# Kernel optimization log

Measured on AMD Instinct MI355X. Metric: run time of the kernel, lower is better.

## Reference

```python
import jax, jax.numpy as jnp
import numpy as np

NUM_HEADS = 8
EPS_OT = 0.05    # self.eps
BETA_T = 1.0     # self.beta_t
N_ITERS = 100    # Sinkhorn max_iter (reference runs all iterations; torch breaks early on convergence)


def setup_inputs() -> dict:
    key = jax.random.key(0)
    ks = jax.random.split(key, 10)
    B, N1, N2 = 16, 256, 576
    dim_t, dim_v, dim_out = 512, 512, 512
    s = 0.02  # conv1d k=1 init scale (stand-in for torch default init)
    f32 = jnp.float32
    return {
        "F_t": jax.random.normal(ks[0], (B, N1, dim_t), f32),
        "F_s": jax.random.normal(ks[1], (B, N2, dim_v), f32),
        # Conv1d(kernel_size=1) weights, squeezed to [out, in]; biases default-on in nn.Conv1d
        "Wq": jax.random.normal(ks[2], (dim_out, dim_t), f32) * s,
        "bq": jnp.zeros((dim_out,), f32),
        "Wk": jax.random.normal(ks[3], (dim_out, dim_v), f32) * s,
        "bk": jnp.zeros((dim_out,), f32),
        "Wv": jax.random.normal(ks[4], (dim_out, dim_v), f32) * s,
        "bv": jnp.zeros((dim_out,), f32),
        "Wp": jax.random.normal(ks[5], (dim_out, dim_out), f32) * s,
        "bp": jnp.zeros((dim_out,), f32),
    }


def sinkhorn_log_exp_sum(C, log_mu, log_nu, eps):
    # C: [BH, N1, N2]; fixed-length log-domain Sinkhorn.
    BH, N1, N2 = C.shape
    u0 = jnp.zeros((BH, N1), C.dtype)
    v0 = jnp.zeros((BH, N2), C.dtype)

    def body(carry, _):
        u, v = carry
        # single K per iteration; both u and v updates use the OLD (u, v), matching torch code
        K = (-C + u[:, :, None] + v[:, None, :]) / eps
        u_new = eps * (log_mu - jax.scipy.special.logsumexp(K, axis=2)) + u
        v_new = eps * (log_nu - jax.scipy.special.logsumexp(K, axis=1)) + v
        return (u_new, v_new), None

    (u, v), _ = jax.lax.scan(jax.checkpoint(body), (u0, v0), None, length=N_ITERS)
    return jnp.exp((-C + u[:, :, None] + v[:, None, :]) / eps)


def _l2norm(x, eps=1e-12):
    return x / jnp.maximum(jnp.linalg.norm(x, axis=-1, keepdims=True), eps)


def reference(F_t, F_s, Wq, bq, Wk, bk, Wv, bv, Wp, bp):
    B, N1, _ = F_t.shape
    N2 = F_s.shape[1]
    H = NUM_HEADS
    dim_out = Wq.shape[0]
    hd = dim_out // H

    # Conv1d(kernel=1) == pointwise linear over channel dim
    q = (F_t @ Wq.T + bq).reshape(B, N1, H, hd)
    k = (F_s @ Wk.T + bk).reshape(B, N2, H, hd)
    v = (F_s @ Wv.T + bv).reshape(B, N2, H, hd)

    q = _l2norm(q)
    k = _l2norm(k)

    sim = jnp.einsum('bnkc,bmkc->bknm', q, k) * BETA_T  # [B,H,N1,N2]
    wdist = (1.0 - sim).reshape(B * H, N1, N2)
    sim_f = sim.reshape(B * H, N1, N2)

    log_mu = jnp.log(jnp.asarray(1.0 / N1 + 1e-8, sim.dtype))
    log_nu = jnp.log(jnp.asarray(1.0 / N2 + 1e-8, sim.dtype))
    T = sinkhorn_log_exp_sum(wdist, log_mu, log_nu, EPS_OT)

    score_map = (N1 * N2 * sim_f * T).reshape(B, H, N1, N2)  # attn_drop = identity (p=0)
    F_t_a = jnp.einsum('bknm,bmkc->bnkc', score_map, v).reshape(B, N1, dim_out)
    F_t_a = F_t_a @ Wp.T + bp
    # torch: F_t_a / F_t_a.norm(dim=-1, keepdim=True)  (plain division, no eps clamp)
    F_t_a = F_t_a / jnp.linalg.norm(F_t_a, axis=-1, keepdims=True)
    return F_t_a  # proj_drop = identity (p=0)
```

## Files before the change

kernel.cpp:

```cpp
#include <hip/hip_runtime.h>
#include <math.h>

#define EPS_OT 0.05f
#define INV_EPS 20.0f

typedef unsigned short ushort_t;
typedef __attribute__((ext_vector_type(8))) short short8;
typedef __attribute__((ext_vector_type(4))) float f32x4;
union Pk { uint4 u; short8 s; };

__device__ __forceinline__ unsigned int f2bf(float f) {
  unsigned int u = __float_as_uint(f);
  return (u + 0x7FFFu + ((u >> 16) & 1u)) >> 16;
}
__device__ __forceinline__ float bf2f(unsigned int u) { return __uint_as_float(u << 16); }

__global__ __launch_bounds__(256) void pack_k(const float* __restrict__ F_t,
                                              const float* __restrict__ F_s,
                                              const float* __restrict__ Wq,
                                              const float* __restrict__ Wk,
                                              const float* __restrict__ Wv,
                                              const float* __restrict__ Wp,
                                              ushort_t* __restrict__ Fth, ushort_t* __restrict__ Ftl,
                                              ushort_t* __restrict__ Fsh, ushort_t* __restrict__ Fsl,
                                              ushort_t* __restrict__ Wqh, ushort_t* __restrict__ Wql,
                                              ushort_t* __restrict__ Wkh, ushort_t* __restrict__ Wkl,
                                              ushort_t* __restrict__ Wvh, ushort_t* __restrict__ Wvl,
                                              ushort_t* __restrict__ Wph) {
  const int blk = blockIdx.x;
  const float* src; ushort_t* dh; ushort_t* dl; size_t off;
  if (blk < 2048)      { src = F_t; dh = Fth; dl = Ftl; off = (size_t)blk * 1024; }
  else if (blk < 6656) { src = F_s; dh = Fsh; dl = Fsl; off = (size_t)(blk - 2048) * 1024; }
  else if (blk < 6912) { src = Wq;  dh = Wqh; dl = Wql; off = (size_t)(blk - 6656) * 1024; }
  else if (blk < 7168) { src = Wk;  dh = Wkh; dl = Wkl; off = (size_t)(blk - 6912) * 1024; }
  else if (blk < 7424) { src = Wv;  dh = Wvh; dl = Wvl; off = (size_t)(blk - 7168) * 1024; }
  else                 { src = Wp;  dh = Wph; dl = nullptr; off = (size_t)(blk - 7424) * 1024; }
  const size_t i = off + (size_t)threadIdx.x * 4;
  float4 f = *(const float4*)(src + i);
  unsigned int h0 = f2bf(f.x), h1 = f2bf(f.y), h2 = f2bf(f.z), h3 = f2bf(f.w);
  uint2 hh; hh.x = h0 | (h1 << 16); hh.y = h2 | (h3 << 16);
  *(uint2*)(dh + i) = hh;
  if (dl) {
    uint2 ll;
    ll.x = f2bf(f.x - bf2f(h0)) | (f2bf(f.y - bf2f(h1)) << 16);
    ll.y = f2bf(f.z - bf2f(h2)) | (f2bf(f.w - bf2f(h3)) << 16);
    *(uint2*)(dl + i) = ll;
  }
}

#define GEMM_HL_BODY()                                                                      \
  f32x4 acc[4] = {};                                                                        \
  for (int k0 = 0; k0 < 512; k0 += 64) {                                                    \
    uint4 a0 = *(const uint4*)(Xp_h + k0), a1 = *(const uint4*)(Xp_h + k0 + 8);             \
    uint4 b0 = *(const uint4*)(Xp_l + k0), b1 = *(const uint4*)(Xp_l + k0 + 8);             \
    uint4 c0 = *(const uint4*)(Wp_h + k0), c1 = *(const uint4*)(Wp_h + k0 + 8);             \
    uint4 d0 = *(const uint4*)(Wp_l + k0), d1 = *(const uint4*)(Wp_l + k0 + 8);             \
    __syncthreads();                                                                        \
    *(uint4*)&Xh[r][cg * 16] = a0; *(uint4*)&Xh[r][cg * 16 + 8] = a1;                       \
    *(uint4*)&Xl[r][cg * 16] = b0; *(uint4*)&Xl[r][cg * 16 + 8] = b1;                       \
    *(uint4*)&Wh[r][cg * 16] = c0; *(uint4*)&Wh[r][cg * 16 + 8] = c1;                       \
    *(uint4*)&Wl[r][cg * 16] = d0; *(uint4*)&Wl[r][cg * 16 + 8] = d1;                       \
    __syncthreads();                                                                        \
    _Pragma("unroll") for (int kst = 0; kst < 2; ++kst) {                                   \
      short8 ah = *(const short8*)&Xh[16 * w + li][kst * 32 + 8 * lg];                      \
      short8 al = *(const short8*)&Xl[16 * w + li][kst * 32 + 8 * lg];                      \
      _Pragma("unroll") for (int nt = 0; nt < 4; ++nt) {                                    \
        short8 bh = *(const short8*)&Wh[nt * 16 + li][kst * 32 + 8 * lg];                   \
        short8 bl = *(const short8*)&Wl[nt * 16 + li][kst * 32 + 8 * lg];                   \
        acc[nt] = __builtin_amdgcn_mfma_f32_16x16x32_bf16(ah, bh, acc[nt], 0, 0, 0);        \
        acc[nt] = __builtin_amdgcn_mfma_f32_16x16x32_bf16(ah, bl, acc[nt], 0, 0, 0);        \
        acc[nt] = __builtin_amdgcn_mfma_f32_16x16x32_bf16(al, bh, acc[nt], 0, 0, 0);        \
      }                                                                                     \
    }                                                                                       \
  }

#define GEMM_PL_BODY()                                                                      \
  f32x4 acc[4] = {};                                                                        \
  for (int k0 = 0; k0 < 512; k0 += 64) {                                                    \
    uint4 a0 = *(const uint4*)(Xp_h + k0), a1 = *(const uint4*)(Xp_h + k0 + 8);             \
    uint4 c0 = *(const uint4*)(Wp_h + k0), c1 = *(const uint4*)(Wp_h + k0 + 8);             \
    __syncthreads();                                                                        \
    *(uint4*)&Xh[r][cg * 16] = a0; *(uint4*)&Xh[r][cg * 16 + 8] = a1;                       \
    *(uint4*)&Wh[r][cg * 16] = c0; *(uint4*)&Wh[r][cg * 16 + 8] = c1;                       \
    __syncthreads();                                                                        \
    _Pragma("unroll") for (int kst = 0; kst < 2; ++kst) {                                   \
      short8 ah = *(const short8*)&Xh[16 * w + li][kst * 32 + 8 * lg];                      \
      _Pragma("unroll") for (int nt = 0; nt < 4; ++nt) {                                    \
        short8 bh = *(const short8*)&Wh[nt * 16 + li][kst * 32 + 8 * lg];                   \
        acc[nt] = __builtin_amdgcn_mfma_f32_16x16x32_bf16(ah, bh, acc[nt], 0, 0, 0);        \
      }                                                                                     \
    }                                                                                       \
  }

__global__ __launch_bounds__(256) void gemmnorm2_k(const ushort_t* __restrict__ Xg_h,
                                                   const ushort_t* __restrict__ Xg_l,
                                                   const ushort_t* __restrict__ Wg_h,
                                                   const ushort_t* __restrict__ Wg_l,
                                                   const float* __restrict__ bias,
                                                   ushort_t* __restrict__ oh,
                                                   ushort_t* __restrict__ ol, int Nn) {
  __shared__ ushort_t Xh[64][72], Xl[64][72], Wh[64][72], Wl[64][72];
  const int tid = threadIdx.x;
  const int w = tid >> 6, l = tid & 63, li = l & 15, lg = l >> 4;
  const int r = tid >> 2, cg = tid & 3;
  const int m0 = blockIdx.x << 6;
  const int h = blockIdx.y, n0 = h << 6;
  const ushort_t* Xp_h = Xg_h + (size_t)(m0 + r) * 512 + cg * 16;
  const ushort_t* Xp_l = Xg_l + (size_t)(m0 + r) * 512 + cg * 16;
  const ushort_t* Wp_h = Wg_h + (size_t)(n0 + r) * 512 + cg * 16;
  const ushort_t* Wp_l = Wg_l + (size_t)(n0 + r) * 512 + cg * 16;
  GEMM_HL_BODY()
  float v[4][4];
  float ss[4] = {0.f, 0.f, 0.f, 0.f};
#pragma unroll
  for (int nt = 0; nt < 4; ++nt) {
    float bb = bias[n0 + nt * 16 + li];
#pragma unroll
    for (int reg = 0; reg < 4; ++reg) {
      float y = acc[nt][reg] + bb;
      v[nt][reg] = y;
      ss[reg] = fmaf(y, y, ss[reg]);
    }
  }
#pragma unroll
  for (int off = 1; off < 16; off <<= 1)
#pragma unroll
    for (int reg = 0; reg < 4; ++reg) ss[reg] += __shfl_xor(ss[reg], off, 64);
  const int b = m0 / Nn;
  const int nbase = m0 - b * Nn;
  const size_t base = ((size_t)(b * 8 + h) * Nn + nbase + 16 * w + 4 * lg) * 64;
#pragma unroll
  for (int reg = 0; reg < 4; ++reg) {
    float inv = 1.0f / fmaxf(sqrtf(ss[reg]), 1e-12f);
#pragma unroll
    for (int nt = 0; nt < 4; ++nt) {
      float y = v[nt][reg] * inv;
      unsigned int hi = f2bf(y);
      size_t idx = base + (size_t)reg * 64 + nt * 16 + li;
      oh[idx] = (ushort_t)hi;
      ol[idx] = (ushort_t)f2bf(y - bf2f(hi));
    }
  }
}

__global__ __launch_bounds__(256) void gemmtrans2_k(const ushort_t* __restrict__ Xg_h,
                                                    const ushort_t* __restrict__ Wg_h,
                                                    const float* __restrict__ bias,
                                                    ushort_t* __restrict__ vt) {
  __shared__ ushort_t Xh[64][72], Wh[64][72];
  __shared__ ushort_t Vs[64 * 73];
  const int tid = threadIdx.x;
  const int w = tid >> 6, l = tid & 63, li = l & 15, lg = l >> 4;
  const int r = tid >> 2, cg = tid & 3;
  const int m0 = blockIdx.x << 6;
  const int h = blockIdx.y, n0 = h << 6;
  const ushort_t* Xp_h = Xg_h + (size_t)(m0 + r) * 512 + cg * 16;
  const ushort_t* Wp_h = Wg_h + (size_t)(n0 + r) * 512 + cg * 16;
  GEMM_PL_BODY()
#pragma unroll
  for (int nt = 0; nt < 4; ++nt) {
    float bb = bias[n0 + nt * 16 + li];
#pragma unroll
    for (int reg = 0; reg < 4; ++reg)
      Vs[(16 * w + 4 * lg + reg) * 73 + nt * 16 + li] = (ushort_t)f2bf(acc[nt][reg] + bb);
  }
  __syncthreads();
  const int a9 = m0 >> 6;
  const int b = a9 / 9;
  const int nbase = m0 - b * 576;
  const int s = b * 8 + h;
  const int c = tid >> 2, q4 = tid & 3;
  ushort_t tmp[16];
#pragma unroll
  for (int jj = 0; jj < 16; ++jj) tmp[jj] = Vs[(q4 * 16 + jj) * 73 + c];
  ushort_t* op = vt + ((size_t)s * 64 + c) * 576 + nbase + q4 * 16;
  *(uint4*)op = *(uint4*)&tmp[0];
  *(uint4*)(op + 8) = *(uint4*)&tmp[8];
}

__global__ __launch_bounds__(256) void gemmplain_k(const ushort_t* __restrict__ Xg_h,
                                                   const ushort_t* __restrict__ Wg_h,
                                                   const float* __restrict__ bias,
                                                   float* __restrict__ Y) {
  __shared__ ushort_t Xh[64][72], Wh[64][72];
  const int tid = threadIdx.x;
  const int w = tid >> 6, l = tid & 63, li = l & 15, lg = l >> 4;
  const int r = tid >> 2, cg = tid & 3;
  const int m0 = blockIdx.x << 6, n0 = blockIdx.y << 6;
  const ushort_t* Xp_h = Xg_h + (size_t)(m0 + r) * 512 + cg * 16;
  const ushort_t* Wp_h = Wg_h + (size_t)(n0 + r) * 512 + cg * 16;
  GEMM_PL_BODY()
#pragma unroll
  for (int nt = 0; nt < 4; ++nt) {
    float bb = bias[n0 + nt * 16 + li];
#pragma unroll
    for (int reg = 0; reg < 4; ++reg)
      Y[(size_t)(m0 + 16 * w + 4 * lg + reg) * 512 + n0 + nt * 16 + li] = acc[nt][reg] + bb;
  }
}

__global__ __launch_bounds__(256) void simE2_k(const ushort_t* __restrict__ qh,
                                               const ushort_t* __restrict__ ql,
                                               const ushort_t* __restrict__ kh,
                                               const ushort_t* __restrict__ kl,
                                               ushort_t* __restrict__ E) {
  const int s = blockIdx.x, i0 = blockIdx.y << 6, j0 = blockIdx.z << 6;
  const int tid = threadIdx.x;
  const int w = tid >> 6, l = tid & 63, li = l & 15, lg = l >> 4;
  const size_t qoff = ((size_t)s * 256 + i0 + 16 * w + li) * 64 + 8 * lg;
  short8 aH0 = *(const short8*)(qh + qoff), aH1 = *(const short8*)(qh + qoff + 32);
  short8 aL0 = *(const short8*)(ql + qoff), aL1 = *(const short8*)(ql + qoff + 32);
  f32x4 acc[4] = {};
#pragma unroll
  for (int nt = 0; nt < 4; ++nt) {
    const size_t koff = ((size_t)s * 576 + j0 + nt * 16 + li) * 64 + 8 * lg;
    short8 bH0 = *(const short8*)(kh + koff), bH1 = *(const short8*)(kh + koff + 32);
    short8 bL0 = *(const short8*)(kl + koff), bL1 = *(const short8*)(kl + koff + 32);
    acc[nt] = __builtin_amdgcn_mfma_f32_16x16x32_bf16(aH0, bH0, acc[nt], 0, 0, 0);
    acc[nt] = __builtin_amdgcn_mfma_f32_16x16x32_bf16(aH1, bH1, acc[nt], 0, 0, 0);
    acc[nt] = __builtin_amdgcn_mfma_f32_16x16x32_bf16(aH0, bL0, acc[nt], 0, 0, 0);
    acc[nt] = __builtin_amdgcn_mfma_f32_16x16x32_bf16(aH1, bL1, acc[nt], 0, 0, 0);
    acc[nt] = __builtin_amdgcn_mfma_f32_16x16x32_bf16(aL0, bH0, acc[nt], 0, 0, 0);
    acc[nt] = __builtin_amdgcn_mfma_f32_16x16x32_bf16(aL1, bH1, acc[nt], 0, 0, 0);
  }
  ushort_t* Ep = E + (size_t)s * 147456;
#pragma unroll
  for (int nt = 0; nt < 4; ++nt)
#pragma unroll
    for (int reg = 0; reg < 4; ++reg) {
      float e = __expf((acc[nt][reg] - 1.0f) * INV_EPS);
      Ep[(size_t)(i0 + 16 * w + 4 * lg + reg) * 576 + j0 + nt * 16 + li] = (ushort_t)f2bf(e);
    }
}

#define SK_SMEM 147456

__global__ __launch_bounds__(1024, 1) void sinkhorn6_k(const ushort_t* __restrict__ E,
                                                       float* __restrict__ gA,
                                                       float* __restrict__ gB,
                                                       unsigned long long* __restrict__ gpart,
                                                       float C_mu, float C_nu) {
  extern __shared__ char smem[];
  const int g = blockIdx.x, s = g >> 1, rh = g & 1, pg = g ^ 1;
  const int tid = threadIdx.x, w = tid >> 6, l = tid & 63, li = l & 15, lg = l >> 4;
  unsigned long long* myP = gpart + (size_t)g * 1152;
  const unsigned long long* prP = gpart + (size_t)pg * 1152;

  ushort_t* Elds = (ushort_t*)smem;
  {
    const uint4* Eg = (const uint4*)(E + (size_t)s * 147456 + (size_t)rh * 73728);
    uint4* El4 = (uint4*)Elds;
    for (int idx = tid; idx < 9216; idx += 1024) El4[idx] = Eg[idx];
  }
  __syncthreads();

  short8 afr[9];
#pragma unroll
  for (int rt = 0; rt < 8; ++rt)
    afr[rt] = *(const short8*)(Elds + (rt * 16 + li) * 576 + w * 32 + 8 * lg);
  const int rtx = w & 7, ktx = 16 + (w >> 3);
  afr[8] = *(const short8*)(Elds + (rtx * 16 + li) * 576 + ktx * 32 + 8 * lg);
  const int ktB = w >> 2, ntb = (w & 3) * 9;
  short8 bfr[9];
#pragma unroll
  for (int p9 = 0; p9 < 9; ++p9) {
    const ushort_t* p = Elds + (ktB * 32 + 8 * lg) * 576 + (ntb + p9) * 16 + li;
    Pk pk;
    pk.u.x = (unsigned int)p[0]    | ((unsigned int)p[576]  << 16);
    pk.u.y = (unsigned int)p[1152] | ((unsigned int)p[1728] << 16);
    pk.u.z = (unsigned int)p[2304] | ((unsigned int)p[2880] << 16);
    pk.u.w = (unsigned int)p[3456] | ((unsigned int)p[4032] << 16);
    bfr[p9] = pk.s;
  }
  __syncthreads();

  float* uu = (float*)smem;
  float* vv = uu + 128;
  unsigned int* au_h = (unsigned int*)(vv + 576);
  unsigned int* au_l = au_h + 64;
  unsigned int* bv_h = au_l + 64;
  unsigned int* bv_l = bv_h + 288;
  float* rpart = (float*)(bv_l + 288);
  float* colp = rpart + 2304;
  float* cso = colp + 2304;
  ushort_t* au_hs = (ushort_t*)au_h;
  ushort_t* au_ls = (ushort_t*)au_l;
  ushort_t* bv_hs = (ushort_t*)bv_h;
  ushort_t* bv_ls = (ushort_t*)bv_l;

  if (tid < 64) { au_h[tid] = 0x3F803F80u; au_l[tid] = 0u; }
  if (tid < 288) { bv_h[tid] = 0x3F803F80u; bv_l[tid] = 0u; }
  __syncthreads();

  for (int t = 0; t < 100; ++t) {
    {
      Pk ah, al;
      ah.u = *(const uint4*)&au_h[ktB * 16 + 4 * lg];
      al.u = *(const uint4*)&au_l[ktB * 16 + 4 * lg];
      float* cp = colp + (w >> 2) * 576;
#pragma unroll
      for (int p9 = 0; p9 < 9; ++p9) {
        f32x4 a2 = {0.f, 0.f, 0.f, 0.f};
        a2 = __builtin_amdgcn_mfma_f32_16x16x32_bf16(ah.s, bfr[p9], a2, 0, 0, 0);
        a2 = __builtin_amdgcn_mfma_f32_16x16x32_bf16(al.s, bfr[p9], a2, 0, 0, 0);
        if (l < 16) cp[(ntb + p9) * 16 + l] = a2[0];
      }
    }
    __syncthreads();
    const int par = t & 1;
    if (tid < 576) {
      float cs = colp[tid] + colp[576 + tid] + colp[1152 + tid] + colp[1728 + tid];
      cso[tid] = cs;
      unsigned long long pv = (unsigned long long)__float_as_uint(cs) |
                              ((unsigned long long)(unsigned int)(t + 1) << 32);
      __hip_atomic_store(&myP[par * 576 + tid], pv, __ATOMIC_RELAXED, __HIP_MEMORY_SCOPE_AGENT);
    }
    {
      Pk bh, bl, bhx, blx;
      bh.u = *(const uint4*)&bv_h[w * 16 + 4 * lg];
      bl.u = *(const uint4*)&bv_l[w * 16 + 4 * lg];
      bhx.u = *(const uint4*)&bv_h[ktx * 16 + 4 * lg];
      blx.u = *(const uint4*)&bv_l[ktx * 16 + 4 * lg];
#pragma unroll
      for (int rt = 0; rt < 8; ++rt) {
        f32x4 a1 = {0.f, 0.f, 0.f, 0.f};
        a1 = __builtin_amdgcn_mfma_f32_16x16x32_bf16(bh.s, afr[rt], a1, 0, 0, 0);
        a1 = __builtin_amdgcn_mfma_f32_16x16x32_bf16(bl.s, afr[rt], a1, 0, 0, 0);
        if (l < 16) rpart[w * 128 + rt * 16 + l] = a1[0];
      }
      f32x4 a1 = {0.f, 0.f, 0.f, 0.f};
      a1 = __builtin_amdgcn_mfma_f32_16x16x32_bf16(bhx.s, afr[8], a1, 0, 0, 0);
      a1 = __builtin_amdgcn_mfma_f32_16x16x32_bf16(blx.s, afr[8], a1, 0, 0, 0);
      if (l < 16) rpart[ktx * 128 + rtx * 16 + l] = a1[0];
    }
    __syncthreads();
    if (tid < 128) {
      float rs = 0.0f;
#pragma unroll
      for (int kc = 0; kc < 18; ++kc) rs += rpart[kc * 128 + tid];
      float un = C_mu - EPS_OT * __logf(rs);
      uu[tid] = un;
      float a = __expf(fminf(fmaxf(un * INV_EPS, -80.f), 80.f));
      unsigned int hi = f2bf(a);
      au_hs[tid] = (ushort_t)hi;
      au_ls[tid] = (ushort_t)f2bf(a - bf2f(hi));
    } else if (tid < 704) {
      const int j = tid - 128;
      const unsigned int tg = (unsigned int)(t + 1);
      unsigned long long p0;
      for (;;) {
        p0 = __hip_atomic_load(&prP[par * 576 + j], __ATOMIC_RELAXED, __HIP_MEMORY_SCOPE_AGENT);
        if ((unsigned int)(p0 >> 32) == tg) break;
        __builtin_amdgcn_s_sleep(1);
      }
      float tot = cso[j] + __uint_as_float((unsigned int)p0);
      float vn = C_nu - EPS_OT * __logf(tot);
      vv[j] = vn;
      float bb = __expf(fminf(fmaxf(vn * INV_EPS, -80.f), 80.f));
      unsigned int hi = f2bf(bb);
      bv_hs[j] = (ushort_t)hi;
      bv_ls[j] = (ushort_t)f2bf(bb - bf2f(hi));
    }
    __syncthreads();
  }
  if (tid < 128) gA[(size_t)s * 256 + rh * 128 + tid] = uu[tid] * INV_EPS;
  if (rh == 0 && tid < 576) gB[(size_t)s * 576 + tid] = vv[tid] * INV_EPS + 11.9012851f;
}

__global__ __launch_bounds__(256) void scorev2_k(const ushort_t* __restrict__ E,
                                                 const ushort_t* __restrict__ vt,
                                                 const float* __restrict__ gA,
                                                 const float* __restrict__ gB,
                                                 ushort_t* __restrict__ Y) {
  __shared__ float gBs[576];
  const int s = blockIdx.x, i0 = blockIdx.y << 6;
  const int tid = threadIdx.x;
  const int w = tid >> 6, l = tid & 63, li = l & 15, lg = l >> 4;
  for (int j = tid; j < 576; j += 256) gBs[j] = gB[(size_t)s * 576 + j];
  const float ga = gA[(size_t)s * 256 + i0 + 16 * w + li];
  const ushort_t* Erow = E + (size_t)s * 147456 + (size_t)(i0 + 16 * w + li) * 576;
  f32x4 acc[4] = {};
  __syncthreads();
  for (int kst = 0; kst < 18; ++kst) {
    const int jb = kst * 32 + 8 * lg;
    Pk eu; eu.u = *(const uint4*)(Erow + jb);
    float pv[8], pl8[8];
#pragma unroll
    for (int jj = 0; jj < 8; ++jj) {
      unsigned int us = (unsigned int)(unsigned short)eu.s[jj];
      float e = bf2f(us);
      float le = __logf(e);
      pv[jj] = (1.0f + EPS_OT * le) * __expf(le + ga + gBs[jb + jj]);
    }
    Pk ph, pl;
#pragma unroll
    for (int jj = 0; jj < 8; ++jj) {
      unsigned int h = f2bf(pv[jj]);
      ((unsigned short*)&ph.s)[jj] = (unsigned short)h;
      pl8[jj] = pv[jj] - bf2f(h);
    }
#pragma unroll
    for (int jj = 0; jj < 8; ++jj)
      ((unsigned short*)&pl.s)[jj] = (unsigned short)f2bf(pl8[jj]);
#pragma unroll
    for (int nt = 0; nt < 4; ++nt) {
      Pk vf; vf.u = *(const uint4*)(vt + ((size_t)s * 64 + nt * 16 + li) * 576 + jb);
      acc[nt] = __builtin_amdgcn_mfma_f32_16x16x32_bf16(ph.s, vf.s, acc[nt], 0, 0, 0);
      acc[nt] = __builtin_amdgcn_mfma_f32_16x16x32_bf16(pl.s, vf.s, acc[nt], 0, 0, 0);
    }
  }
  const int b = s >> 3, h = s & 7;
#pragma unroll
  for (int nt = 0; nt < 4; ++nt)
#pragma unroll
    for (int reg = 0; reg < 4; ++reg)
      Y[((size_t)(b * 256 + i0 + 16 * w + 4 * lg + reg) << 9) + (h << 6) + nt * 16 + li] =
          (ushort_t)f2bf(acc[nt][reg]);
}

__global__ __launch_bounds__(256) void rownorm_k(const float* __restrict__ X,
                                                 float* __restrict__ out) {
  const size_t row = blockIdx.x;
  const int tid = threadIdx.x;
  float x0 = X[(row << 9) + tid], x1 = X[(row << 9) + 256 + tid];
  float st = fmaf(x0, x0, x1 * x1);
#pragma unroll
  for (int off = 32; off; off >>= 1) st += __shfl_xor(st, off, 64);
  __shared__ float ps[4];
  if ((tid & 63) == 0) ps[tid >> 6] = st;
  __syncthreads();
  const float inv = 1.0f / sqrtf(ps[0] + ps[1] + ps[2] + ps[3]);
  out[(row << 9) + tid] = x0 * inv;
  out[(row << 9) + 256 + tid] = x1 * inv;
}

extern "C" void kernel_launch(void* const* d_in, const int* in_sizes, int n_in,
                              void* d_out, int out_size, void* d_ws, size_t ws_size,
                              hipStream_t stream) {
  const float* F_t = (const float*)d_in[0];
  const float* F_s = (const float*)d_in[1];
  const float* Wq = (const float*)d_in[2];
  const float* bq = (const float*)d_in[3];
  const float* Wk = (const float*)d_in[4];
  const float* bk = (const float*)d_in[5];
  const float* Wv = (const float*)d_in[6];
  const float* bvb = (const float*)d_in[7];
  const float* Wp = (const float*)d_in[8];
  const float* bp = (const float*)d_in[9];
  float* out = (float*)d_out;

  ushort_t* u0 = (ushort_t*)d_ws;
  ushort_t* Fth = u0;
  ushort_t* Ftl = Fth + 2097152;
  ushort_t* Fsh = Ftl + 2097152;
  ushort_t* Fsl = Fsh + 4718592;
  ushort_t* Wqh = Fsl + 4718592;
  ushort_t* Wql = Wqh + 262144;
  ushort_t* Wkh = Wql + 262144;
  ushort_t* Wkl = Wkh + 262144;
  ushort_t* Wvh = Wkl + 262144;
  ushort_t* Wvl = Wvh + 262144;
  ushort_t* Wph = Wvl + 262144;
  ushort_t* qh = Wph + 262144;
  ushort_t* ql = qh + 2097152;
  ushort_t* kh = ql + 2097152;
  ushort_t* kl = kh + 4718592;
  ushort_t* vt = kl + 4718592;
  ushort_t* Eb = vt + 4718592;
  ushort_t* T0b = Eb + 18874368;
  float* T1 = (float*)(T0b + 2097152);
  float* gA = T1 + 2097152;
  float* gB = gA + 32768;
  unsigned long long* gpart = (unsigned long long*)(gB + 73728);

  const float C_mu = (float)(0.05 * log(1.0 / 256.0 + 1e-8));
  const float C_nu = (float)(0.05 * log(1.0 / 576.0 + 1e-8));

  (void)hipFuncSetAttribute((const void*)sinkhorn6_k,
                            hipFuncAttributeMaxDynamicSharedMemorySize, SK_SMEM);

  pack_k<<<7680, 256, 0, stream>>>(F_t, F_s, Wq, Wk, Wv, Wp, Fth, Ftl, Fsh, Fsl,
                                   Wqh, Wql, Wkh, Wkl, Wvh, Wvl, Wph);
  gemmnorm2_k<<<dim3(64, 8), 256, 0, stream>>>(Fth, Ftl, Wqh, Wql, bq, qh, ql, 256);
  gemmnorm2_k<<<dim3(144, 8), 256, 0, stream>>>(Fsh, Fsl, Wkh, Wkl, bk, kh, kl, 576);
  gemmtrans2_k<<<dim3(144, 8), 256, 0, stream>>>(Fsh, Wvh, bvb, vt);
  simE2_k<<<dim3(128, 4, 9), 256, 0, stream>>>(qh, ql, kh, kl, Eb);
  sinkhorn6_k<<<256, 1024, SK_SMEM, stream>>>(Eb, gA, gB, gpart, C_mu, C_nu);
  scorev2_k<<<dim3(128, 4), 256, 0, stream>>>(Eb, vt, gA, gB, T0b);
  gemmplain_k<<<dim3(64, 8), 256, 0, stream>>>(T0b, Wph, bp, T1);
  rownorm_k<<<4096, 256, 0, stream>>>(T1, out);
}
```

Measured before the change: 430.3 us.

## Fuse similarity, Sinkhorn and score-V into one persistent kernel

```diff
diff --git a/kernel.cpp b/kernel.cpp
--- a/kernel.cpp
+++ b/kernel.cpp
@@ -199,60 +199,67 @@
   }
 }
 
-__global__ __launch_bounds__(256) void simE2_k(const ushort_t* __restrict__ qh,
-                                               const ushort_t* __restrict__ ql,
-                                               const ushort_t* __restrict__ kh,
-                                               const ushort_t* __restrict__ kl,
-                                               ushort_t* __restrict__ E) {
-  const int s = blockIdx.x, i0 = blockIdx.y << 6, j0 = blockIdx.z << 6;
-  const int tid = threadIdx.x;
-  const int w = tid >> 6, l = tid & 63, li = l & 15, lg = l >> 4;
-  const size_t qoff = ((size_t)s * 256 + i0 + 16 * w + li) * 64 + 8 * lg;
-  short8 aH0 = *(const short8*)(qh + qoff), aH1 = *(const short8*)(qh + qoff + 32);
-  short8 aL0 = *(const short8*)(ql + qoff), aL1 = *(const short8*)(ql + qoff + 32);
-  f32x4 acc[4] = {};
-#pragma unroll
-  for (int nt = 0; nt < 4; ++nt) {
-    const size_t koff = ((size_t)s * 576 + j0 + nt * 16 + li) * 64 + 8 * lg;
-    short8 bH0 = *(const short8*)(kh + koff), bH1 = *(const short8*)(kh + koff + 32);
-    short8 bL0 = *(const short8*)(kl + koff), bL1 = *(const short8*)(kl + koff + 32);
-    acc[nt] = __builtin_amdgcn_mfma_f32_16x16x32_bf16(aH0, bH0, acc[nt], 0, 0, 0);
-    acc[nt] = __builtin_amdgcn_mfma_f32_16x16x32_bf16(aH1, bH1, acc[nt], 0, 0, 0);
-    acc[nt] = __builtin_amdgcn_mfma_f32_16x16x32_bf16(aH0, bL0, acc[nt], 0, 0, 0);
-    acc[nt] = __builtin_amdgcn_mfma_f32_16x16x32_bf16(aH1, bL1, acc[nt], 0, 0, 0);
-    acc[nt] = __builtin_amdgcn_mfma_f32_16x16x32_bf16(aL0, bH0, acc[nt], 0, 0, 0);
-    acc[nt] = __builtin_amdgcn_mfma_f32_16x16x32_bf16(aL1, bH1, acc[nt], 0, 0, 0);
-  }
-  ushort_t* Ep = E + (size_t)s * 147456;
-#pragma unroll
-  for (int nt = 0; nt < 4; ++nt)
-#pragma unroll
-    for (int reg = 0; reg < 4; ++reg) {
-      float e = __expf((acc[nt][reg] - 1.0f) * INV_EPS);
-      Ep[(size_t)(i0 + 16 * w + 4 * lg + reg) * 576 + j0 + nt * 16 + li] = (ushort_t)f2bf(e);
-    }
-}
-
-#define SK_SMEM 147456
-
-__global__ __launch_bounds__(1024, 1) void sinkhorn6_k(const ushort_t* __restrict__ E,
-                                                       float* __restrict__ gA,
-                                                       float* __restrict__ gB,
+#define SK7_SMEM 155648
+
+__global__ __launch_bounds__(1024, 1) void sinkhorn7_k(const ushort_t* __restrict__ qh,
+                                                       const ushort_t* __restrict__ ql,
+                                                       const ushort_t* __restrict__ kh,
+                                                       const ushort_t* __restrict__ kl,
+                                                       const ushort_t* __restrict__ vt,
+                                                       ushort_t* __restrict__ Y,
                                                        unsigned long long* __restrict__ gpart,
                                                        float C_mu, float C_nu) {
   extern __shared__ char smem[];
+  ushort_t* Elds = (ushort_t*)smem;
+  char* scr = smem + 147456;
+  ushort_t* khs = (ushort_t*)scr;
+  ushort_t* kls = khs + 2048;
+  float* uu = (float*)scr;
+  float* vv = uu + 128;
+  float* rsum = vv + 576;
+  float* colsum = rsum + 128;
+  ushort_t* au = (ushort_t*)(colsum + 576);
+  ushort_t* bv = au + 128;
+
   const int g = blockIdx.x, s = g >> 1, rh = g & 1, pg = g ^ 1;
   const int tid = threadIdx.x, w = tid >> 6, l = tid & 63, li = l & 15, lg = l >> 4;
   unsigned long long* myP = gpart + (size_t)g * 1152;
   const unsigned long long* prP = gpart + (size_t)pg * 1152;
 
-  ushort_t* Elds = (ushort_t*)smem;
-  {
-    const uint4* Eg = (const uint4*)(E + (size_t)s * 147456 + (size_t)rh * 73728);
-    uint4* El4 = (uint4*)Elds;
-    for (int idx = tid; idx < 9216; idx += 1024) El4[idx] = Eg[idx];
-  }
-  __syncthreads();
+  const int it = w & 7, ntp = w >> 3;
+  const size_t qoff = ((size_t)(s * 256 + rh * 128 + it * 16 + li)) * 64 + 8 * lg;
+  short8 aH0 = *(const short8*)(qh + qoff), aH1 = *(const short8*)(qh + qoff + 32);
+  short8 aL0 = *(const short8*)(ql + qoff), aL1 = *(const short8*)(ql + qoff + 32);
+
+  for (int jt = 0; jt < 9; ++jt) {
+#pragma unroll
+    for (int p = 0; p < 2; ++p) {
+      const int q = tid & 511;
+      const int jr = jt * 64 + p * 32 + (q >> 4);
+      const size_t src = ((size_t)(s * 576 + jr)) * 64 + (q & 15) * 4;
+      if (tid < 512) ((uint2*)khs)[q] = *(const uint2*)(kh + src);
+      else           ((uint2*)kls)[q] = *(const uint2*)(kl + src);
+      __syncthreads();
+      const ushort_t* kb_h = khs + (ntp * 16 + li) * 64 + 8 * lg;
+      const ushort_t* kb_l = kls + (ntp * 16 + li) * 64 + 8 * lg;
+      short8 bH0 = *(const short8*)kb_h, bH1 = *(const short8*)(kb_h + 32);
+      short8 bL0 = *(const short8*)kb_l, bL1 = *(const short8*)(kb_l + 32);
+      f32x4 acc = {0.f, 0.f, 0.f, 0.f};
+      acc = __builtin_amdgcn_mfma_f32_16x16x32_bf16(aH0, bH0, acc, 0, 0, 0);
+      acc = __builtin_amdgcn_mfma_f32_16x16x32_bf16(aH1, bH1, acc, 0, 0, 0);
+      acc = __builtin_amdgcn_mfma_f32_16x16x32_bf16(aH0, bL0, acc, 0, 0, 0);
+      acc = __builtin_amdgcn_mfma_f32_16x16x32_bf16(aH1, bL1, acc, 0, 0, 0);
+      acc = __builtin_amdgcn_mfma_f32_16x16x32_bf16(aL0, bH0, acc, 0, 0, 0);
+      acc = __builtin_amdgcn_mfma_f32_16x16x32_bf16(aL1, bH1, acc, 0, 0, 0);
+#pragma unroll
+      for (int reg = 0; reg < 4; ++reg) {
+        float e = __expf((acc[reg] - 1.0f) * INV_EPS);
+        Elds[(it * 16 + 4 * lg + reg) * 576 + jt * 64 + p * 32 + ntp * 16 + li] =
+            (ushort_t)f2bf(e);
+      }
+      __syncthreads();
+    }
+  }
 
   short8 afr[9];
 #pragma unroll
@@ -272,150 +279,108 @@
     pk.u.w = (unsigned int)p[3456] | ((unsigned int)p[4032] << 16);
     bfr[p9] = pk.s;
   }
+  if (tid < 128) { uu[tid] = 0.0f; au[tid] = (ushort_t)0x3F80; rsum[tid] = 0.0f; }
+  if (tid < 576) { vv[tid] = 0.0f; bv[tid] = (ushort_t)0x3F80; colsum[tid] = 0.0f; }
   __syncthreads();
 
-  float* uu = (float*)smem;
-  float* vv = uu + 128;
-  unsigned int* au_h = (unsigned int*)(vv + 576);
-  unsigned int* au_l = au_h + 64;
-  unsigned int* bv_h = au_l + 64;
-  unsigned int* bv_l = bv_h + 288;
-  float* rpart = (float*)(bv_l + 288);
-  float* colp = rpart + 2304;
-  float* cso = colp + 2304;
-  ushort_t* au_hs = (ushort_t*)au_h;
-  ushort_t* au_ls = (ushort_t*)au_l;
-  ushort_t* bv_hs = (ushort_t*)bv_h;
-  ushort_t* bv_ls = (ushort_t*)bv_l;
-
-  if (tid < 64) { au_h[tid] = 0x3F803F80u; au_l[tid] = 0u; }
-  if (tid < 288) { bv_h[tid] = 0x3F803F80u; bv_l[tid] = 0u; }
-  __syncthreads();
-
   for (int t = 0; t < 100; ++t) {
+    if (tid < 128) rsum[tid] = 0.0f;
     {
-      Pk ah, al;
-      ah.u = *(const uint4*)&au_h[ktB * 16 + 4 * lg];
-      al.u = *(const uint4*)&au_l[ktB * 16 + 4 * lg];
-      float* cp = colp + (w >> 2) * 576;
+      Pk ah; ah.u = *(const uint4*)(au + ktB * 32 + 8 * lg);
 #pragma unroll
       for (int p9 = 0; p9 < 9; ++p9) {
         f32x4 a2 = {0.f, 0.f, 0.f, 0.f};
         a2 = __builtin_amdgcn_mfma_f32_16x16x32_bf16(ah.s, bfr[p9], a2, 0, 0, 0);
-        a2 = __builtin_amdgcn_mfma_f32_16x16x32_bf16(al.s, bfr[p9], a2, 0, 0, 0);
-        if (l < 16) cp[(ntb + p9) * 16 + l] = a2[0];
+        if (l < 16) atomicAdd(&colsum[(ntb + p9) * 16 + l], a2[0]);
       }
     }
     __syncthreads();
     const int par = t & 1;
+    float csMine = 0.0f;
     if (tid < 576) {
-      float cs = colp[tid] + colp[576 + tid] + colp[1152 + tid] + colp[1728 + tid];
-      cso[tid] = cs;
-      unsigned long long pv = (unsigned long long)__float_as_uint(cs) |
+      csMine = colsum[tid];
+      unsigned long long pv = (unsigned long long)__float_as_uint(csMine) |
                               ((unsigned long long)(unsigned int)(t + 1) << 32);
       __hip_atomic_store(&myP[par * 576 + tid], pv, __ATOMIC_RELAXED, __HIP_MEMORY_SCOPE_AGENT);
     }
     {
-      Pk bh, bl, bhx, blx;
-      bh.u = *(const uint4*)&bv_h[w * 16 + 4 * lg];
-      bl.u = *(const uint4*)&bv_l[w * 16 + 4 * lg];
-      bhx.u = *(const uint4*)&bv_h[ktx * 16 + 4 * lg];
-      blx.u = *(const uint4*)&bv_l[ktx * 16 + 4 * lg];
+      Pk bh, bhx;
+      bh.u = *(const uint4*)(bv + w * 32 + 8 * lg);
+      bhx.u = *(const uint4*)(bv + ktx * 32 + 8 * lg);
 #pragma unroll
       for (int rt = 0; rt < 8; ++rt) {
         f32x4 a1 = {0.f, 0.f, 0.f, 0.f};
         a1 = __builtin_amdgcn_mfma_f32_16x16x32_bf16(bh.s, afr[rt], a1, 0, 0, 0);
-        a1 = __builtin_amdgcn_mfma_f32_16x16x32_bf16(bl.s, afr[rt], a1, 0, 0, 0);
-        if (l < 16) rpart[w * 128 + rt * 16 + l] = a1[0];
+        if (l < 16) atomicAdd(&rsum[rt * 16 + l], a1[0]);
       }
       f32x4 a1 = {0.f, 0.f, 0.f, 0.f};
       a1 = __builtin_amdgcn_mfma_f32_16x16x32_bf16(bhx.s, afr[8], a1, 0, 0, 0);
-      a1 = __builtin_amdgcn_mfma_f32_16x16x32_bf16(blx.s, afr[8], a1, 0, 0, 0);
-      if (l < 16) rpart[ktx * 128 + rtx * 16 + l] = a1[0];
+      if (l < 16) atomicAdd(&rsum[rtx * 16 + l], a1[0]);
     }
     __syncthreads();
-    if (tid < 128) {
-      float rs = 0.0f;
-#pragma unroll
-      for (int kc = 0; kc < 18; ++kc) rs += rpart[kc * 128 + tid];
-      float un = C_mu - EPS_OT * __logf(rs);
-      uu[tid] = un;
-      float a = __expf(fminf(fmaxf(un * INV_EPS, -80.f), 80.f));
-      unsigned int hi = f2bf(a);
-      au_hs[tid] = (ushort_t)hi;
-      au_ls[tid] = (ushort_t)f2bf(a - bf2f(hi));
-    } else if (tid < 704) {
-      const int j = tid - 128;
+    if (tid < 576) {
       const unsigned int tg = (unsigned int)(t + 1);
       unsigned long long p0;
       for (;;) {
-        p0 = __hip_atomic_load(&prP[par * 576 + j], __ATOMIC_RELAXED, __HIP_MEMORY_SCOPE_AGENT);
+        p0 = __hip_atomic_load(&prP[par * 576 + tid], __ATOMIC_RELAXED, __HIP_MEMORY_SCOPE_AGENT);
         if ((unsigned int)(p0 >> 32) == tg) break;
         __builtin_amdgcn_s_sleep(1);
       }
-      float tot = cso[j] + __uint_as_float((unsigned int)p0);
-      float vn = C_nu - EPS_OT * __logf(tot);
-      vv[j] = vn;
-      float bb = __expf(fminf(fmaxf(vn * INV_EPS, -80.f), 80.f));
-      unsigned int hi = f2bf(bb);
-      bv_hs[j] = (ushort_t)hi;
-      bv_ls[j] = (ushort_t)f2bf(bb - bf2f(hi));
+      float vn = C_nu - EPS_OT * __logf(csMine + __uint_as_float((unsigned int)p0));
+      vv[tid] = vn;
+      bv[tid] = (ushort_t)f2bf(__expf(fminf(fmaxf(vn * INV_EPS, -80.f), 80.f)));
+    } else if (tid < 704) {
+      const int i = tid - 576;
+      float un = C_mu - EPS_OT * __logf(rsum[i]);
+      uu[i] = un;
+      au[i] = (ushort_t)f2bf(__expf(fminf(fmaxf(un * INV_EPS, -80.f), 80.f)));
+    } else {
+      for (int j = tid - 704; j < 576; j += 320) colsum[j] = 0.0f;
     }
     __syncthreads();
   }
-  if (tid < 128) gA[(size_t)s * 256 + rh * 128 + tid] = uu[tid] * INV_EPS;
-  if (rh == 0 && tid < 576) gB[(size_t)s * 576 + tid] = vv[tid] * INV_EPS + 11.9012851f;
-}
-
-__global__ __launch_bounds__(256) void scorev2_k(const ushort_t* __restrict__ E,
-                                                 const ushort_t* __restrict__ vt,
-                                                 const float* __restrict__ gA,
-                                                 const float* __restrict__ gB,
-                                                 ushort_t* __restrict__ Y) {
-  __shared__ float gBs[576];
-  const int s = blockIdx.x, i0 = blockIdx.y << 6;
-  const int tid = threadIdx.x;
-  const int w = tid >> 6, l = tid & 63, li = l & 15, lg = l >> 4;
-  for (int j = tid; j < 576; j += 256) gBs[j] = gB[(size_t)s * 576 + j];
-  const float ga = gA[(size_t)s * 256 + i0 + 16 * w + li];
-  const ushort_t* Erow = E + (size_t)s * 147456 + (size_t)(i0 + 16 * w + li) * 576;
-  f32x4 acc[4] = {};
+
+  if (tid < 576) vv[tid] = vv[tid] * INV_EPS + 11.9012851f;
   __syncthreads();
-  for (int kst = 0; kst < 18; ++kst) {
-    const int jb = kst * 32 + 8 * lg;
-    Pk eu; eu.u = *(const uint4*)(Erow + jb);
-    float pv[8], pl8[8];
-#pragma unroll
-    for (int jj = 0; jj < 8; ++jj) {
-      unsigned int us = (unsigned int)(unsigned short)eu.s[jj];
-      float e = bf2f(us);
-      float le = __logf(e);
-      pv[jj] = (1.0f + EPS_OT * le) * __expf(le + ga + gBs[jb + jj]);
-    }
-    Pk ph, pl;
-#pragma unroll
-    for (int jj = 0; jj < 8; ++jj) {
-      unsigned int h = f2bf(pv[jj]);
-      ((unsigned short*)&ph.s)[jj] = (unsigned short)h;
-      pl8[jj] = pv[jj] - bf2f(h);
-    }
-#pragma unroll
-    for (int jj = 0; jj < 8; ++jj)
-      ((unsigned short*)&pl.s)[jj] = (unsigned short)f2bf(pl8[jj]);
-#pragma unroll
-    for (int nt = 0; nt < 4; ++nt) {
-      Pk vf; vf.u = *(const uint4*)(vt + ((size_t)s * 64 + nt * 16 + li) * 576 + jb);
-      acc[nt] = __builtin_amdgcn_mfma_f32_16x16x32_bf16(ph.s, vf.s, acc[nt], 0, 0, 0);
-      acc[nt] = __builtin_amdgcn_mfma_f32_16x16x32_bf16(pl.s, vf.s, acc[nt], 0, 0, 0);
-    }
-  }
-  const int b = s >> 3, h = s & 7;
-#pragma unroll
-  for (int nt = 0; nt < 4; ++nt)
-#pragma unroll
-    for (int reg = 0; reg < 4; ++reg)
-      Y[((size_t)(b * 256 + i0 + 16 * w + 4 * lg + reg) << 9) + (h << 6) + nt * 16 + li] =
-          (ushort_t)f2bf(acc[nt][reg]);
+  {
+    const float ga = uu[it * 16 + li] * INV_EPS;
+    const int nt0 = ntp * 2, nt1 = nt0 + 1;
+    const ushort_t* Erow = Elds + (it * 16 + li) * 576;
+    const ushort_t* v0p = vt + ((size_t)s * 64 + nt0 * 16 + li) * 576;
+    const ushort_t* v1p = vt + ((size_t)s * 64 + nt1 * 16 + li) * 576;
+    f32x4 oa0 = {0.f, 0.f, 0.f, 0.f}, oa1 = {0.f, 0.f, 0.f, 0.f};
+    for (int kst = 0; kst < 18; ++kst) {
+      const int jb = kst * 32 + 8 * lg;
+      Pk eu; eu.u = *(const uint4*)(Erow + jb);
+      float pv[8];
+#pragma unroll
+      for (int jj = 0; jj < 8; ++jj) {
+        float e = bf2f((unsigned int)(unsigned short)eu.s[jj]);
+        float le = __logf(e);
+        pv[jj] = (1.0f + EPS_OT * le) * __expf(le + ga + vv[jb + jj]);
+      }
+      Pk ph, pl;
+#pragma unroll
+      for (int jj = 0; jj < 8; ++jj) {
+        unsigned int hb = f2bf(pv[jj]);
+        ((unsigned short*)&ph.s)[jj] = (unsigned short)hb;
+        ((unsigned short*)&pl.s)[jj] = (unsigned short)f2bf(pv[jj] - bf2f(hb));
+      }
+      Pk v0; v0.u = *(const uint4*)(v0p + jb);
+      Pk v1; v1.u = *(const uint4*)(v1p + jb);
+      oa0 = __builtin_amdgcn_mfma_f32_16x16x32_bf16(ph.s, v0.s, oa0, 0, 0, 0);
+      oa0 = __builtin_amdgcn_mfma_f32_16x16x32_bf16(pl.s, v0.s, oa0, 0, 0, 0);
+      oa1 = __builtin_amdgcn_mfma_f32_16x16x32_bf16(ph.s, v1.s, oa1, 0, 0, 0);
+      oa1 = __builtin_amdgcn_mfma_f32_16x16x32_bf16(pl.s, v1.s, oa1, 0, 0, 0);
+    }
+    const int b = s >> 3, h = s & 7;
+    const int orow = b * 256 + rh * 128 + it * 16 + 4 * lg;
+#pragma unroll
+    for (int reg = 0; reg < 4; ++reg) {
+      Y[((size_t)(orow + reg) << 9) + h * 64 + nt0 * 16 + li] = (ushort_t)f2bf(oa0[reg]);
+      Y[((size_t)(orow + reg) << 9) + h * 64 + nt1 * 16 + li] = (ushort_t)f2bf(oa1[reg]);
+    }
+  }
 }
 
 __global__ __launch_bounds__(256) void rownorm_k(const float* __restrict__ X,
@@ -466,27 +431,22 @@
   ushort_t* kh = ql + 2097152;
   ushort_t* kl = kh + 4718592;
   ushort_t* vt = kl + 4718592;
-  ushort_t* Eb = vt + 4718592;
-  ushort_t* T0b = Eb + 18874368;
+  ushort_t* T0b = vt + 4718592;
   float* T1 = (float*)(T0b + 2097152);
-  float* gA = T1 + 2097152;
-  float* gB = gA + 32768;
-  unsigned long long* gpart = (unsigned long long*)(gB + 73728);
+  unsigned long long* gpart = (unsigned long long*)(T1 + 2097152);
 
   const float C_mu = (float)(0.05 * log(1.0 / 256.0 + 1e-8));
   const float C_nu = (float)(0.05 * log(1.0 / 576.0 + 1e-8));
 
-  (void)hipFuncSetAttribute((const void*)sinkhorn6_k,
-                            hipFuncAttributeMaxDynamicSharedMemorySize, SK_SMEM);
+  (void)hipFuncSetAttribute((const void*)sinkhorn7_k,
+                            hipFuncAttributeMaxDynamicSharedMemorySize, SK7_SMEM);
 
   pack_k<<<7680, 256, 0, stream>>>(F_t, F_s, Wq, Wk, Wv, Wp, Fth, Ftl, Fsh, Fsl,
                                    Wqh, Wql, Wkh, Wkl, Wvh, Wvl, Wph);
   gemmnorm2_k<<<dim3(64, 8), 256, 0, stream>>>(Fth, Ftl, Wqh, Wql, bq, qh, ql, 256);
   gemmnorm2_k<<<dim3(144, 8), 256, 0, stream>>>(Fsh, Fsl, Wkh, Wkl, bk, kh, kl, 576);
   gemmtrans2_k<<<dim3(144, 8), 256, 0, stream>>>(Fsh, Wvh, bvb, vt);
-  simE2_k<<<dim3(128, 4, 9), 256, 0, stream>>>(qh, ql, kh, kl, Eb);
-  sinkhorn6_k<<<256, 1024, SK_SMEM, stream>>>(Eb, gA, gB, gpart, C_mu, C_nu);
-  scorev2_k<<<dim3(128, 4), 256, 0, stream>>>(Eb, vt, gA, gB, T0b);
+  sinkhorn7_k<<<256, 1024, SK7_SMEM, stream>>>(qh, ql, kh, kl, vt, T0b, gpart, C_mu, C_nu);
   gemmplain_k<<<dim3(64, 8), 256, 0, stream>>>(T0b, Wph, bp, T1);
   rownorm_k<<<4096, 256, 0, stream>>>(T1, out);
 }
```

After: 874.8 us. 103% more time.
